# Kernel tuning notes

Hardware: AMD Instinct MI355X
Metric: run time of the kernel (lower is better)

Reference implementation:

```python
import jax, jax.numpy as jnp
import numpy as np

B = 16; H = 64; W = 64; DIM = 512; HEADS = 8; WS = 8; SS = 4; HID = 2048
HD = DIM // HEADS; SC = HD ** -0.5; N = WS * WS; NW = (H // WS) * (W // WS)


def _rel_pos_index():
    coords = np.stack(np.meshgrid(np.arange(WS), np.arange(WS), indexing='ij'))
    cf = coords.reshape(2, -1)
    rel = (cf[:, :, None] - cf[:, None, :]).transpose(1, 2, 0).copy()
    rel[:, :, 0] += WS - 1
    rel[:, :, 1] += WS - 1
    rel[:, :, 0] *= 2 * WS - 1
    return rel.sum(-1).reshape(-1)  # (N*N,)


def _attn_mask():
    # standard Swin shifted-window mask: 0 within region, -100 across regions
    img = np.zeros((H, W))
    cnt = 0
    for hs in (slice(0, -WS), slice(-WS, -SS), slice(-SS, None)):
        for ws_ in (slice(0, -WS), slice(-WS, -SS), slice(-SS, None)):
            img[hs, ws_] = cnt
            cnt += 1
    mw = img.reshape(H // WS, WS, W // WS, WS).transpose(0, 2, 1, 3).reshape(-1, N)
    d = mw[:, None, :] - mw[:, :, None]
    return np.where(d != 0, -100.0, 0.0).astype(np.float32)  # (NW, N, N)

RPI = jnp.asarray(_rel_pos_index())
MASK = jnp.asarray(_attn_mask())


def _win_part(x):  # (b,H,W,C) -> (b*NW, N, C)
    b = x.shape[0]
    return x.reshape(b, H // WS, WS, W // WS, WS, DIM).transpose(0, 1, 3, 2, 4, 5).reshape(-1, N, DIM)


def _win_rev(w, b):  # (b*NW, N, C) -> (b,H,W,C)
    return w.reshape(b, H // WS, W // WS, WS, WS, DIM).transpose(0, 1, 3, 2, 4, 5).reshape(b, H, W, DIM)


def _mlp(x, w1, b1, w2, b2):
    return jax.nn.relu(x @ w1 + b1) @ w2 + b2


def setup_inputs() -> dict:
    key = jax.random.key(0)
    ks = jax.random.split(key, 40)
    def n(i, shape, s=0.02):
        return jax.random.normal(ks[i], shape, dtype=jnp.float32) * s
    inp = {
        'x': jax.random.normal(ks[0], (B, H * W, DIM), dtype=jnp.float32),
        'scale': jax.random.normal(ks[1], (B, H * W, DIM), dtype=jnp.float32),
        'shift': jax.random.normal(ks[2], (B, H * W, DIM), dtype=jnp.float32),
    }
    for i, nm in enumerate(['wq', 'wk', 'wv', 'wvs', 'wvh', 'wpx', 'wps', 'wph']):
        inp[nm] = n(3 + i, (DIM, DIM))
        inp['b' + nm[1:]] = jnp.zeros((DIM,), jnp.float32)
    inp['rpb_table'] = n(20, ((2 * WS - 1) * (2 * WS - 1), HEADS))
    for j, sfx in enumerate(['x', 's', 'h']):
        inp['w1' + sfx] = n(21 + j, (DIM, HID))
        inp['b1' + sfx] = jnp.zeros((HID,), jnp.float32)
        inp['w2' + sfx] = n(24 + j, (HID, DIM))
        inp['b2' + sfx] = jnp.zeros((DIM,), jnp.float32)
    return inp


def reference(x, scale, shift, wq, bq, wk, bk, wv, bv, wvs, bvs, wvh, bvh,
              wpx, bpx, wps, bps, wph, bph, rpb_table,
              w1x, b1x, w2x, b2x, w1s, b1s, w2s, b2s, w1h, b1h, w2h, b2h):
    b = x.shape[0]

    def to_win(t):  # cyclic shift then window partition
        t = jnp.roll(t.reshape(b, H, W, DIM), (-SS, -SS), (1, 2))
        return _win_part(t)

    xw, sw, hw = to_win(x), to_win(scale), to_win(shift)
    B_ = xw.shape[0]

    def heads(t, w, bb):
        return (t @ w + bb).reshape(B_, N, HEADS, HD).transpose(0, 2, 1, 3)

    q = heads(xw, wq, bq) * SC
    k = heads(xw, wk, bk)
    v = heads(xw, wv, bv)
    vs = heads(sw, wvs, bvs)
    vh = heads(hw, wvh, bvh)

    attn = jnp.einsum('bhnd,bhmd->bhnm', q, k)  # (B_, HEADS, N, N)
    rpb = rpb_table[RPI].reshape(N, N, HEADS).transpose(2, 0, 1)
    attn = attn + rpb[None]
    attn = (attn.reshape(B_ // NW, NW, HEADS, N, N) + MASK[None, :, None]).reshape(B_, HEADS, N, N)
    attn = jax.nn.softmax(attn, axis=-1)

    def out(v_, wp, bp):
        o = jnp.einsum('bhnm,bhmd->bhnd', attn, v_).transpose(0, 2, 1, 3).reshape(B_, N, DIM)
        return o @ wp + bp

    def from_win(t):  # window reverse then reverse cyclic shift
        return jnp.roll(_win_rev(t, b), (SS, SS), (1, 2)).reshape(b, H * W, DIM)

    x = x + from_win(out(v, wpx, bpx))
    scale = scale + from_win(out(vs, wps, bps))
    shift = shift + from_win(out(vh, wph, bph))

    x = x + _mlp(x, w1x, b1x, w2x, b2x)
    scale = scale + _mlp(scale, w1s, b1s, w2s, b2s)
    shift = shift + _mlp(shift, w1h, b1h, w2h, b2h)
    return (x, scale, shift)
```

## Files before the change

### kernel.cpp

```cpp
#include <hip/hip_runtime.h>


typedef unsigned short u16;
typedef unsigned int   u32;
typedef __attribute__((ext_vector_type(8))) short shortx8;
typedef __attribute__((ext_vector_type(4))) float floatx4;

__device__ __forceinline__ u16 f2bu(float f) {
  u32 b = __builtin_bit_cast(u32, f);
  b += 0x7fffu + ((b >> 16) & 1u);
  return (u16)(b >> 16);
}
__device__ __forceinline__ float bu2f(u32 lo16) {
  u32 b = (lo16 & 0xffffu) << 16;
  return __builtin_bit_cast(float, b);
}
__device__ __forceinline__ u32 pk2(float a, float b) {
  return (u32)f2bu(a) | ((u32)f2bu(b) << 16);
}
__device__ __forceinline__ uint4 pack8(float4 a, float4 b) {
  uint4 u;
  u.x = pk2(a.x, a.y); u.y = pk2(a.z, a.w);
  u.z = pk2(b.x, b.y); u.w = pk2(b.z, b.w);
  return u;
}
__device__ __forceinline__ int gmap(int t) {
  int win = t >> 6, n = t & 63;
  int b = win >> 6, wy = (win >> 3) & 7, wx = win & 7;
  int r = (wy * 8 + (n >> 3) + 4) & 63;
  int c = (wx * 8 + (n & 7) + 4) & 63;
  return (b << 12) + (r << 6) + c;
}

__global__ void transpose_cvt(const float* __restrict__ src, u16* __restrict__ dst,
                              int K, int N) {
  __shared__ float tile[32][33];
  int n0 = blockIdx.x * 32, k0 = blockIdx.y * 32;
  int tx = threadIdx.x, ty = threadIdx.y;
#pragma unroll
  for (int i = 0; i < 32; i += 8)
    tile[ty + i][tx] = src[(size_t)(k0 + ty + i) * N + n0 + tx];
  __syncthreads();
#pragma unroll
  for (int i = 0; i < 32; i += 8)
    dst[(size_t)(n0 + ty + i) * K + k0 + tx] = f2bu(tile[tx][ty + i]);
}

template <int AMODE, int EPI>
__global__ __launch_bounds__(256) void gemm_k(
    const void* __restrict__ Aany, int lda,
    const u16* __restrict__ Bt, int K,
    const float* __restrict__ bias0, const float* __restrict__ bias1,
    const float* __restrict__ resid,
    float* __restrict__ outf,
    u16* __restrict__ outb0, u16* __restrict__ outb1) {
  __shared__ __align__(16) u16 lA[128][72];
  __shared__ __align__(16) u16 lB[128][72];
  const int tid = threadIdx.x;
  const int lane = tid & 63;
  const int wv = tid >> 6;
  const int wm = wv >> 1, wn = wv & 1;
  const int m16 = lane & 15, qd = lane >> 4;
  const int row0 = blockIdx.y * 128;
  const int col0 = blockIdx.x * 128;
  const int sr = tid >> 1;
  const int sc = (tid & 1) << 5;

  size_t aoff;
  if constexpr (AMODE == 0) aoff = (size_t)gmap(row0 + sr) * lda;
  else                      aoff = (size_t)(row0 + sr) * lda;
  const float* af = (const float*)Aany;
  const u16*   ab = (const u16*)Aany;
  const u16* brow = Bt + (size_t)(col0 + sr) * K;

  floatx4 acc[4][4];
#pragma unroll
  for (int i = 0; i < 4; ++i)
#pragma unroll
    for (int j = 0; j < 4; ++j)
#pragma unroll
      for (int r = 0; r < 4; ++r) acc[i][j][r] = 0.f;

  for (int k0 = 0; k0 < K; k0 += 64) {
    if constexpr (AMODE <= 1) {
      const float* p = af + aoff + k0 + sc;
      float4 f0 = *(const float4*)(p + 0);
      float4 f1 = *(const float4*)(p + 4);
      float4 f2 = *(const float4*)(p + 8);
      float4 f3 = *(const float4*)(p + 12);
      *(uint4*)&lA[sr][sc + 0] = pack8(f0, f1);
      *(uint4*)&lA[sr][sc + 8] = pack8(f2, f3);
      f0 = *(const float4*)(p + 16);
      f1 = *(const float4*)(p + 20);
      f2 = *(const float4*)(p + 24);
      f3 = *(const float4*)(p + 28);
      *(uint4*)&lA[sr][sc + 16] = pack8(f0, f1);
      *(uint4*)&lA[sr][sc + 24] = pack8(f2, f3);
    } else {
      const u16* p = ab + aoff + k0 + sc;
      *(uint4*)&lA[sr][sc + 0]  = *(const uint4*)(p + 0);
      *(uint4*)&lA[sr][sc + 8]  = *(const uint4*)(p + 8);
      *(uint4*)&lA[sr][sc + 16] = *(const uint4*)(p + 16);
      *(uint4*)&lA[sr][sc + 24] = *(const uint4*)(p + 24);
    }
    {
      const u16* p = brow + k0 + sc;
      *(uint4*)&lB[sr][sc + 0]  = *(const uint4*)(p + 0);
      *(uint4*)&lB[sr][sc + 8]  = *(const uint4*)(p + 8);
      *(uint4*)&lB[sr][sc + 16] = *(const uint4*)(p + 16);
      *(uint4*)&lB[sr][sc + 24] = *(const uint4*)(p + 24);
    }
    __syncthreads();
#pragma unroll
    for (int kk = 0; kk < 64; kk += 32) {
      shortx8 a[4], b[4];
#pragma unroll
      for (int i = 0; i < 4; ++i)
        a[i] = *(const shortx8*)&lA[wm * 64 + i * 16 + m16][kk + qd * 8];
#pragma unroll
      for (int j = 0; j < 4; ++j)
        b[j] = *(const shortx8*)&lB[wn * 64 + j * 16 + m16][kk + qd * 8];
#pragma unroll
      for (int i = 0; i < 4; ++i)
#pragma unroll
        for (int j = 0; j < 4; ++j)
          acc[i][j] = __builtin_amdgcn_mfma_f32_16x16x32_bf16(a[i], b[j], acc[i][j], 0, 0, 0);
    }
    __syncthreads();
  }

#pragma unroll
  for (int i = 0; i < 4; ++i) {
#pragma unroll
    for (int j = 0; j < 4; ++j) {
#pragma unroll
      for (int rr = 0; rr < 4; ++rr) {
        int row = row0 + wm * 64 + i * 16 + qd * 4 + rr;
        int col = col0 + wn * 64 + j * 16 + m16;
        float v = acc[i][j][rr];
        if constexpr (EPI == 0) {
          int mat = col >> 9, cc = col & 511;
          float val = mat == 0 ? (v + bias0[cc]) * 0.125f : (v + bias1[cc]);
          int win = row >> 6, n = row & 63, hh = cc >> 6, dd = cc & 63;
          size_t dst = (((size_t)(win * 8 + hh) * 64 + n) * 64) + dd;
          (mat ? outb1 : outb0)[dst] = f2bu(val);
        } else if constexpr (EPI == 1) {
          float val = v + bias0[col];
          int win = row >> 6, n = row & 63, hh = col >> 6, dd = col & 63;
          outb0[(((size_t)(win * 8 + hh) * 64 + n) * 64) + dd] = f2bu(val);
        } else if constexpr (EPI == 2) {
          float val = v + bias0[col];
          size_t g = (size_t)gmap(row) * 512 + col;
          outf[g] = resid[g] + val;
        } else if constexpr (EPI == 3) {
          float val = fmaxf(v + bias0[col], 0.f);
          outb0[(size_t)row * 2048 + col] = f2bu(val);
        } else {
          float val = v + bias0[col];
          size_t idx = (size_t)row * 512 + col;
          outf[idx] += val;
        }
      }
    }
  }
}

__global__ __launch_bounds__(256) void attn_softmax(
    const u16* __restrict__ Qb, const u16* __restrict__ Kb,
    const float* __restrict__ rpb, u16* __restrict__ Pb) {
  __shared__ float lq[64][65], lk[64][65], S[64][65];
  __shared__ float rmax[64], rsum[64];
  int bid = blockIdx.x;
  int h = bid & 7, winb = (bid >> 3) & 63;
  int tid = threadIdx.x;
  int r = tid >> 2, q4 = tid & 3;

  const u16* qt = Qb + (size_t)bid * 4096 + r * 64 + q4 * 16;
  const u16* kt = Kb + (size_t)bid * 4096 + r * 64 + q4 * 16;
  uint4 a0 = *(const uint4*)qt, a1 = *(const uint4*)(qt + 8);
  uint4 b0 = *(const uint4*)kt, b1 = *(const uint4*)(kt + 8);
  {
    float* d = &lq[r][q4 * 16];
    d[0] = bu2f(a0.x); d[1] = bu2f(a0.x >> 16); d[2] = bu2f(a0.y); d[3] = bu2f(a0.y >> 16);
    d[4] = bu2f(a0.z); d[5] = bu2f(a0.z >> 16); d[6] = bu2f(a0.w); d[7] = bu2f(a0.w >> 16);
    d[8] = bu2f(a1.x); d[9] = bu2f(a1.x >> 16); d[10] = bu2f(a1.y); d[11] = bu2f(a1.y >> 16);
    d[12] = bu2f(a1.z); d[13] = bu2f(a1.z >> 16); d[14] = bu2f(a1.w); d[15] = bu2f(a1.w >> 16);
    float* e = &lk[r][q4 * 16];
    e[0] = bu2f(b0.x); e[1] = bu2f(b0.x >> 16); e[2] = bu2f(b0.y); e[3] = bu2f(b0.y >> 16);
    e[4] = bu2f(b0.z); e[5] = bu2f(b0.z >> 16); e[6] = bu2f(b0.w); e[7] = bu2f(b0.w >> 16);
    e[8] = bu2f(b1.x); e[9] = bu2f(b1.x >> 16); e[10] = bu2f(b1.y); e[11] = bu2f(b1.y >> 16);
    e[12] = bu2f(b1.z); e[13] = bu2f(b1.z >> 16); e[14] = bu2f(b1.w); e[15] = bu2f(b1.w >> 16);
  }
  __syncthreads();

  int n = r, mb = q4 * 16;
  float sv[16];
#pragma unroll
  for (int mm = 0; mm < 16; ++mm) sv[mm] = 0.f;
  for (int kk = 0; kk < 64; ++kk) {
    float qv = lq[n][kk];
#pragma unroll
    for (int mm = 0; mm < 16; ++mm) sv[mm] += qv * lk[mb + mm][kk];
  }
  int wy = winb >> 3, wx = winb & 7;
  int grn = wy * 8 + (n >> 3), gcn = wx * 8 + (n & 7);
  int ridn = (grn < 56 ? 0 : (grn < 60 ? 1 : 2)) * 3 + (gcn < 56 ? 0 : (gcn < 60 ? 1 : 2));
#pragma unroll
  for (int mm = 0; mm < 16; ++mm) {
    int m = mb + mm;
    int dy = (n >> 3) - (m >> 3) + 7, dx = (n & 7) - (m & 7) + 7;
    float bias = rpb[(dy * 15 + dx) * 8 + h];
    int grm = wy * 8 + (m >> 3), gcm = wx * 8 + (m & 7);
    int ridm = (grm < 56 ? 0 : (grm < 60 ? 1 : 2)) * 3 + (gcm < 56 ? 0 : (gcm < 60 ? 1 : 2));
    S[n][m] = sv[mm] + bias + (ridm == ridn ? 0.f : -100.f);
  }
  __syncthreads();
  if (tid < 64) {
    float mx = -1e30f;
    for (int m = 0; m < 64; ++m) mx = fmaxf(mx, S[tid][m]);
    float sum = 0.f;
    for (int m = 0; m < 64; ++m) sum += __expf(S[tid][m] - mx);
    rmax[tid] = mx; rsum[tid] = 1.f / sum;
  }
  __syncthreads();
  float mx = rmax[r], is = rsum[r];
  float p[16];
#pragma unroll
  for (int i = 0; i < 16; ++i) p[i] = __expf(S[r][mb + i] - mx) * is;
  uint4 o0, o1;
  o0.x = pk2(p[0], p[1]); o0.y = pk2(p[2], p[3]); o0.z = pk2(p[4], p[5]); o0.w = pk2(p[6], p[7]);
  o1.x = pk2(p[8], p[9]); o1.y = pk2(p[10], p[11]); o1.z = pk2(p[12], p[13]); o1.w = pk2(p[14], p[15]);
  u16* dst = Pb + (size_t)bid * 4096 + r * 64 + mb;
  *(uint4*)dst = o0; *(uint4*)(dst + 8) = o1;
}

__global__ __launch_bounds__(256) void attn_av(
    const u16* __restrict__ Pb, const u16* __restrict__ Vb, u16* __restrict__ Ob) {
  __shared__ float lP[64][68], lv[64][68];
  int bid = blockIdx.x;
  int win = bid >> 3, h = bid & 7;
  int tid = threadIdx.x, r = tid >> 2, q4 = tid & 3;

  const u16* pt = Pb + (size_t)bid * 4096 + r * 64 + q4 * 16;
  const u16* vt = Vb + (size_t)bid * 4096 + r * 64 + q4 * 16;
  uint4 a0 = *(const uint4*)pt, a1 = *(const uint4*)(pt + 8);
  uint4 b0 = *(const uint4*)vt, b1 = *(const uint4*)(vt + 8);
  {
    float4* f = (float4*)&lP[r][q4 * 16];
    f[0] = make_float4(bu2f(a0.x), bu2f(a0.x >> 16), bu2f(a0.y), bu2f(a0.y >> 16));
    f[1] = make_float4(bu2f(a0.z), bu2f(a0.z >> 16), bu2f(a0.w), bu2f(a0.w >> 16));
    f[2] = make_float4(bu2f(a1.x), bu2f(a1.x >> 16), bu2f(a1.y), bu2f(a1.y >> 16));
    f[3] = make_float4(bu2f(a1.z), bu2f(a1.z >> 16), bu2f(a1.w), bu2f(a1.w >> 16));
    float4* g = (float4*)&lv[r][q4 * 16];
    g[0] = make_float4(bu2f(b0.x), bu2f(b0.x >> 16), bu2f(b0.y), bu2f(b0.y >> 16));
    g[1] = make_float4(bu2f(b0.z), bu2f(b0.z >> 16), bu2f(b0.w), bu2f(b0.w >> 16));
    g[2] = make_float4(bu2f(b1.x), bu2f(b1.x >> 16), bu2f(b1.y), bu2f(b1.y >> 16));
    g[3] = make_float4(bu2f(b1.z), bu2f(b1.z >> 16), bu2f(b1.w), bu2f(b1.w >> 16));
  }
  __syncthreads();

  int n = r, db = q4 * 16;
  float acc[16];
#pragma unroll
  for (int i = 0; i < 16; ++i) acc[i] = 0.f;
  for (int m = 0; m < 64; ++m) {
    float p = lP[n][m];
    const float4* vp = (const float4*)&lv[m][db];
    float4 v0 = vp[0], v1 = vp[1], v2 = vp[2], v3 = vp[3];
    acc[0] += p * v0.x; acc[1] += p * v0.y; acc[2] += p * v0.z; acc[3] += p * v0.w;
    acc[4] += p * v1.x; acc[5] += p * v1.y; acc[6] += p * v1.z; acc[7] += p * v1.w;
    acc[8] += p * v2.x; acc[9] += p * v2.y; acc[10] += p * v2.z; acc[11] += p * v2.w;
    acc[12] += p * v3.x; acc[13] += p * v3.y; acc[14] += p * v3.z; acc[15] += p * v3.w;
  }
  uint4 o0, o1;
  o0.x = pk2(acc[0], acc[1]); o0.y = pk2(acc[2], acc[3]);
  o0.z = pk2(acc[4], acc[5]); o0.w = pk2(acc[6], acc[7]);
  o1.x = pk2(acc[8], acc[9]); o1.y = pk2(acc[10], acc[11]);
  o1.z = pk2(acc[12], acc[13]); o1.w = pk2(acc[14], acc[15]);
  u16* dst = Ob + ((size_t)(win * 64 + n)) * 512 + h * 64 + db;
  *(uint4*)dst = o0; *(uint4*)(dst + 8) = o1;
}

extern "C" void kernel_launch(void* const* d_in, const int* in_sizes, int n_in,
                              void* d_out, int out_size, void* d_ws, size_t ws_size,
                              hipStream_t stream) {
  (void)in_sizes; (void)n_in; (void)out_size; (void)ws_size;
  const float* xin[3] = {(const float*)d_in[0], (const float*)d_in[1], (const float*)d_in[2]};
  const float* bq = (const float*)d_in[4];
  const float* bk = (const float*)d_in[6];
  const float* bv[3] = {(const float*)d_in[8], (const float*)d_in[10], (const float*)d_in[12]};
  const float* bp[3] = {(const float*)d_in[14], (const float*)d_in[16], (const float*)d_in[18]};
  const float* rpb = (const float*)d_in[19];
  const float* b1[3] = {(const float*)d_in[21], (const float*)d_in[25], (const float*)d_in[29]};
  const float* b2[3] = {(const float*)d_in[23], (const float*)d_in[27], (const float*)d_in[31]};
  float* dout = (float*)d_out;
  u16* wsb = (u16*)d_ws;

  const int   tsrc[14] = {3, 5, 7, 9, 11, 13, 15, 17, 20, 24, 28, 22, 26, 30};
  const size_t tdst[14] = {0, 262144, 524288, 786432, 1048576, 1310720, 1572864, 1835008,
                           2097152, 3145728, 4194304, 5242880, 6291456, 7340032};
  const int   tK[14] = {512, 512, 512, 512, 512, 512, 512, 512, 512, 512, 512, 2048, 2048, 2048};
  const int   tN[14] = {512, 512, 512, 512, 512, 512, 512, 512, 2048, 2048, 2048, 512, 512, 512};
  for (int i = 0; i < 14; ++i)
    transpose_cvt<<<dim3(tN[i] / 32, tK[i] / 32), dim3(32, 8), 0, stream>>>(
        (const float*)d_in[tsrc[i]], wsb + tdst[i], tK[i], tN[i]);

  u16* Wqk = wsb;
  u16* Wv[3] = {wsb + 524288, wsb + 786432, wsb + 1048576};
  u16* Wp[3] = {wsb + 1310720, wsb + 1572864, wsb + 1835008};
  u16* W1[3] = {wsb + 2097152, wsb + 3145728, wsb + 4194304};
  u16* W2[3] = {wsb + 5242880, wsb + 6291456, wsb + 7340032};
  u16* Qb = wsb + 8388608;
  u16* Kb = wsb + 41943040;
  u16* Pb = wsb + 75497472;
  u16* Vb = Qb;
  u16* Ob = Kb;
  u16* Hb = wsb + 8388608;

  gemm_k<0, 0><<<dim3(8, 512), 256, 0, stream>>>(xin[0], 512, Wqk, 512, bq, bk,
                                                 nullptr, nullptr, Qb, Kb);
  attn_softmax<<<dim3(8192), 256, 0, stream>>>(Qb, Kb, rpb, Pb);

  for (int s = 0; s < 3; ++s) {
    gemm_k<0, 1><<<dim3(4, 512), 256, 0, stream>>>(xin[s], 512, Wv[s], 512, bv[s],
                                                   nullptr, nullptr, nullptr, Vb, nullptr);
    attn_av<<<dim3(8192), 256, 0, stream>>>(Pb, Vb, Ob);
    gemm_k<2, 2><<<dim3(4, 512), 256, 0, stream>>>(Ob, 512, Wp[s], 512, bp[s], nullptr,
                                                   xin[s], dout + (size_t)s * 33554432,
                                                   nullptr, nullptr);
  }
  for (int s = 0; s < 3; ++s) {
    for (int c = 0; c < 2; ++c) {
      float* dO = dout + (size_t)s * 33554432 + (size_t)c * 16777216;
      gemm_k<1, 3><<<dim3(16, 256), 256, 0, stream>>>(dO, 512, W1[s], 512, b1[s],
                                                      nullptr, nullptr, nullptr, Hb, nullptr);
      gemm_k<2, 4><<<dim3(4, 256), 256, 0, stream>>>(Hb, 2048, W2[s], 2048, b2[s],
                                                     nullptr, nullptr, dO, nullptr, nullptr);
    }
  }
}
```

Measured before the change: 3.881 ms.

## Use direct global-to-LDS loads, swizzled block order, and bf16 proj output for MLP

Bf16 operand tiles now go straight from global memory into LDS through the global_load_lds builtin, and the B tile drops its padding. Blocks are remapped with an XCD-aware swizzle on a 1D grid to improve L2 locality. The projection epilogue also writes a bf16 window-ordered copy of the residual output, so the MLP's first GEMM reads bf16 instead of converting fp32, and the second GEMM scatters back through gmap with a row offset in 4 chunks. Unpadded LDS rows may cause bank conflicts on MFMA fragment reads, and the extra bf16 write adds store traffic.

```diff
diff --git a/kernel.cpp b/kernel.cpp
--- a/kernel.cpp
+++ b/kernel.cpp
@@ -32,6 +32,12 @@
   return (b << 12) + (r << 6) + c;
 }
 
+__device__ __forceinline__ void gload16(const void* g, void* l) {
+  __builtin_amdgcn_global_load_lds(
+      (const __attribute__((address_space(1))) void*)g,
+      (__attribute__((address_space(3))) void*)l, 16, 0, 0);
+}
+
 __global__ void transpose_cvt(const float* __restrict__ src, u16* __restrict__ dst,
                               int K, int N) {
   __shared__ float tile[32][33];
@@ -46,32 +52,38 @@
     dst[(size_t)(n0 + ty + i) * K + k0 + tx] = f2bu(tile[tx][ty + i]);
 }
 
-template <int AMODE, int EPI>
+template <int AMODE, int EPI, int NBX>
 __global__ __launch_bounds__(256) void gemm_k(
     const void* __restrict__ Aany, int lda,
     const u16* __restrict__ Bt, int K,
     const float* __restrict__ bias0, const float* __restrict__ bias1,
     const float* __restrict__ resid,
     float* __restrict__ outf,
-    u16* __restrict__ outb0, u16* __restrict__ outb1) {
-  __shared__ __align__(16) u16 lA[128][72];
-  __shared__ __align__(16) u16 lB[128][72];
+    u16* __restrict__ outb0, u16* __restrict__ outb1, int rowoff) {
+  constexpr int LDA = (AMODE == 0) ? 72 : 64;
+  __shared__ __align__(16) u16 lA[128][LDA];
+  __shared__ __align__(16) u16 lB[128][64];
   const int tid = threadIdx.x;
   const int lane = tid & 63;
   const int wv = tid >> 6;
   const int wm = wv >> 1, wn = wv & 1;
   const int m16 = lane & 15, qd = lane >> 4;
-  const int row0 = blockIdx.y * 128;
-  const int col0 = blockIdx.x * 128;
+
+  const int nwg = gridDim.x;
+  const int lid = ((blockIdx.x & 7) * (nwg >> 3)) + (blockIdx.x >> 3);
+  const int by = lid / NBX, bx = lid - by * NBX;
+  const int row0 = by * 128, col0 = bx * 128;
+
+  const u16* bsrc = Bt + (size_t)(col0 + wv * 32 + (lane >> 3)) * K + (lane & 7) * 8;
+
+  const float* af = (const float*)Aany;
+  const u16*   ab = (const u16*)Aany;
   const int sr = tid >> 1;
   const int sc = (tid & 1) << 5;
-
-  size_t aoff;
+  size_t aoff = 0;
+  const u16* asrc = nullptr;
   if constexpr (AMODE == 0) aoff = (size_t)gmap(row0 + sr) * lda;
-  else                      aoff = (size_t)(row0 + sr) * lda;
-  const float* af = (const float*)Aany;
-  const u16*   ab = (const u16*)Aany;
-  const u16* brow = Bt + (size_t)(col0 + sr) * K;
+  else asrc = ab + (size_t)(row0 + wv * 32 + (lane >> 3)) * lda + (lane & 7) * 8;
 
   floatx4 acc[4][4];
 #pragma unroll
@@ -82,7 +94,7 @@
       for (int r = 0; r < 4; ++r) acc[i][j][r] = 0.f;
 
   for (int k0 = 0; k0 < K; k0 += 64) {
-    if constexpr (AMODE <= 1) {
+    if constexpr (AMODE == 0) {
       const float* p = af + aoff + k0 + sc;
       float4 f0 = *(const float4*)(p + 0);
       float4 f1 = *(const float4*)(p + 4);
@@ -97,19 +109,13 @@
       *(uint4*)&lA[sr][sc + 16] = pack8(f0, f1);
       *(uint4*)&lA[sr][sc + 24] = pack8(f2, f3);
     } else {
-      const u16* p = ab + aoff + k0 + sc;
-      *(uint4*)&lA[sr][sc + 0]  = *(const uint4*)(p + 0);
-      *(uint4*)&lA[sr][sc + 8]  = *(const uint4*)(p + 8);
-      *(uint4*)&lA[sr][sc + 16] = *(const uint4*)(p + 16);
-      *(uint4*)&lA[sr][sc + 24] = *(const uint4*)(p + 24);
+#pragma unroll
+      for (int t = 0; t < 4; ++t)
+        gload16(asrc + (size_t)(k0 + t * 8 * lda), &lA[wv * 32 + t * 8][0]);
     }
-    {
-      const u16* p = brow + k0 + sc;
-      *(uint4*)&lB[sr][sc + 0]  = *(const uint4*)(p + 0);
-      *(uint4*)&lB[sr][sc + 8]  = *(const uint4*)(p + 8);
-      *(uint4*)&lB[sr][sc + 16] = *(const uint4*)(p + 16);
-      *(uint4*)&lB[sr][sc + 24] = *(const uint4*)(p + 24);
-    }
+#pragma unroll
+    for (int t = 0; t < 4; ++t)
+      gload16(bsrc + (size_t)(k0 + t * 8 * K), &lB[wv * 32 + t * 8][0]);
     __syncthreads();
 #pragma unroll
     for (int kk = 0; kk < 64; kk += 32) {
@@ -151,14 +157,16 @@
         } else if constexpr (EPI == 2) {
           float val = v + bias0[col];
           size_t g = (size_t)gmap(row) * 512 + col;
-          outf[g] = resid[g] + val;
+          float y = resid[g] + val;
+          outf[g] = y;
+          outb0[(size_t)row * 512 + col] = f2bu(y);
         } else if constexpr (EPI == 3) {
           float val = fmaxf(v + bias0[col], 0.f);
           outb0[(size_t)row * 2048 + col] = f2bu(val);
         } else {
           float val = v + bias0[col];
-          size_t idx = (size_t)row * 512 + col;
-          outf[idx] += val;
+          size_t g = (size_t)gmap(row + rowoff) * 512 + col;
+          outf[g] += val;
         }
       }
     }
@@ -315,27 +323,28 @@
   u16* Pb = wsb + 75497472;
   u16* Vb = Qb;
   u16* Ob = Kb;
-  u16* Hb = wsb + 8388608;
-
-  gemm_k<0, 0><<<dim3(8, 512), 256, 0, stream>>>(xin[0], 512, Wqk, 512, bq, bk,
-                                                 nullptr, nullptr, Qb, Kb);
+  u16* Yb = Qb;
+  u16* Hb = Kb;
+
+  gemm_k<0, 0, 8><<<4096, 256, 0, stream>>>(xin[0], 512, Wqk, 512, bq, bk,
+                                            nullptr, nullptr, Qb, Kb, 0);
   attn_softmax<<<dim3(8192), 256, 0, stream>>>(Qb, Kb, rpb, Pb);
 
   for (int s = 0; s < 3; ++s) {
-    gemm_k<0, 1><<<dim3(4, 512), 256, 0, stream>>>(xin[s], 512, Wv[s], 512, bv[s],
-                                                   nullptr, nullptr, nullptr, Vb, nullptr);
+    gemm_k<0, 1, 4><<<2048, 256, 0, stream>>>(xin[s], 512, Wv[s], 512, bv[s],
+                                              nullptr, nullptr, nullptr, Vb, nullptr, 0);
     attn_av<<<dim3(8192), 256, 0, stream>>>(Pb, Vb, Ob);
-    gemm_k<2, 2><<<dim3(4, 512), 256, 0, stream>>>(Ob, 512, Wp[s], 512, bp[s], nullptr,
-                                                   xin[s], dout + (size_t)s * 33554432,
-                                                   nullptr, nullptr);
-  }
-  for (int s = 0; s < 3; ++s) {
-    for (int c = 0; c < 2; ++c) {
-      float* dO = dout + (size_t)s * 33554432 + (size_t)c * 16777216;
-      gemm_k<1, 3><<<dim3(16, 256), 256, 0, stream>>>(dO, 512, W1[s], 512, b1[s],
-                                                      nullptr, nullptr, nullptr, Hb, nullptr);
-      gemm_k<2, 4><<<dim3(4, 256), 256, 0, stream>>>(Hb, 2048, W2[s], 2048, b2[s],
-                                                     nullptr, nullptr, dO, nullptr, nullptr);
+    gemm_k<2, 2, 4><<<2048, 256, 0, stream>>>(Ob, 512, Wp[s], 512, bp[s], nullptr,
+                                              xin[s], dout + (size_t)s * 33554432,
+                                              Yb, nullptr, 0);
+    for (int c = 0; c < 4; ++c) {
+      const u16* Ac = Yb + (size_t)c * 8388608;
+      gemm_k<2, 3, 16><<<2048, 256, 0, stream>>>(Ac, 512, W1[s], 512, b1[s],
+                                                 nullptr, nullptr, nullptr, Hb, nullptr, 0);
+      gemm_k<2, 4, 4><<<512, 256, 0, stream>>>(Hb, 2048, W2[s], 2048, b2[s],
+                                               nullptr, nullptr,
+                                               dout + (size_t)s * 33554432,
+                                               nullptr, nullptr, c * 16384);
     }
   }
 }
```

New measurement: 3.659 ms. 1.06x faster.
